# Performance work log

Hardware: AMD Instinct MI355X
Metric: run time of the kernel (lower is better)

Reference implementation:

```python
import jax, jax.numpy as jnp
import numpy as np

TAU = 1.0  # forward() default temperature

def setup_inputs() -> dict:
    key = jax.random.key(0)
    ks = jax.random.split(key, 6)
    B, T, I, H, O = 1024, 512, 100, 150, 3
    s_ih = 1.0 / np.sqrt(H)  # torch nn.RNN init scale (uniform +-1/sqrt(H)); randn used for simplicity of magnitude
    return {
        "x": jax.random.normal(ks[0], (B, T, I), dtype=jnp.float32),
        "h0": jax.random.normal(ks[1], (B, H), dtype=jnp.float32),  # init=True: h ~ N(0,1)
        "g": jax.random.normal(ks[2], (B, T, O), dtype=jnp.float32),  # gumbel noise (externalized)
        "W_ih": jax.random.normal(ks[3], (H, I), dtype=jnp.float32) * s_ih,
        "W_hh": jax.random.normal(ks[4], (H, H), dtype=jnp.float32) * s_ih,
        "W_fc": jax.random.normal(ks[5], (O, H), dtype=jnp.float32) * s_ih,
    }

def _rnn_relu(x, h0, W_ih, W_hh):
    # x: [B,T,I]; precompute input projection once (batched GEMM), then scan over time.
    xw = jnp.einsum("bti,hi->tbh", x, W_ih)  # [T,B,H]
    def step(h, xw_t):
        h = jax.nn.relu(xw_t + h @ W_hh.T)
        return h, h
    _, hs = jax.lax.scan(step, h0, xw)  # hs: [T,B,H]
    return jnp.transpose(hs, (1, 0, 2))  # [B,T,H]

def reference(x, h0, g, W_ih, W_hh, W_fc):
    hidden = _rnn_relu(x, h0, W_ih, W_hh)           # [B,T,H]
    logits = jnp.einsum("bth,oh->bto", hidden, W_fc)  # [B,T,O]
    # F.gumbel_softmax(hard=True): softmax((logits+g)/tau), straight-through one-hot
    y_soft = jax.nn.softmax((logits + g) / TAU, axis=-1)
    idx = jnp.argmax(y_soft, axis=-1)
    y_hard = jax.nn.one_hot(idx, logits.shape[-1], dtype=y_soft.dtype)
    out = y_soft + jax.lax.stop_gradient(y_hard - y_soft)
    return (out, hidden, logits)
```

## Files before the change

### kernel.cpp

```cpp
#include <hip/hip_runtime.h>

constexpr int NB = 1024;
constexpr int NT = 512;
constexpr int NI = 100;
constexpr int NH = 150;
constexpr int NO = 3;
constexpr int KP = 256;
constexpr int XOFF = 152;
constexpr int ROWS = 4;
constexpr int NCH = 8;

__global__ __launch_bounds__(512, 2)
void rnn_fused(const float* __restrict__ x, const float* __restrict__ h0,
               const float* __restrict__ g, const float* __restrict__ Wih,
               const float* __restrict__ Whh, const float* __restrict__ Wfc,
               float* __restrict__ out, float* __restrict__ hidden,
               float* __restrict__ logits)
{
    __shared__ __align__(16) float hx[ROWS * KP];
    __shared__ float lgt[ROWS][4];

    const int tid  = threadIdx.x;
    const int lane = tid & 63;
    const int wv   = tid >> 6;
    const int kg   = lane & 7;
    const int oq   = lane >> 3;
    const int oi   = wv * 8 + oq;
    const int row0 = blockIdx.x * ROWS;

    float Wreg[3][NCH][4];
#pragma unroll
    for (int j = 0; j < 3; ++j) {
        const int o = oi + 64 * j;
#pragma unroll
        for (int i = 0; i < NCH; ++i) {
#pragma unroll
            for (int q = 0; q < 4; ++q) {
                const int k = 4 * (kg + 8 * i) + q;
                float v = 0.f;
                if (o < NH) {
                    if (k < NH) v = Whh[o * NH + k];
                    else if (k >= XOFF && k < XOFF + NI) v = Wih[o * NI + (k - XOFF)];
                } else if (o < NH + NO) {
                    if (k < NH) v = Wfc[(o - NH) * NH + k];
                }
                Wreg[j][i][q] = v;
            }
        }
    }

    for (int e = tid; e < ROWS * NH; e += 512) {
        int b = e / NH, k = e - b * NH;
        hx[b * KP + k] = h0[(row0 + b) * NH + k];
    }
    for (int e = tid; e < ROWS * NI; e += 512) {
        int b = e / NI, i = e - b * NI;
        hx[b * KP + XOFF + i] = x[((size_t)(row0 + b) * NT + 0) * NI + i];
    }
    if (tid < ROWS * 6) {
        int b = tid / 6, z = tid - b * 6;
        int k = (z < 2) ? (NH + z) : (252 + z - 2);
        hx[b * KP + k] = 0.f;
    }
    __syncthreads();

    const float4* hx4 = reinterpret_cast<const float4*>(hx);
    const int xb = tid / 25, xq = tid - xb * 25;

    for (int t = 0; t <= NT; ++t) {
        float4 xp = make_float4(0.f, 0.f, 0.f, 0.f);
        if (tid < 100 && t < NT - 1) {
            xp = *reinterpret_cast<const float4*>(
                &x[((size_t)(row0 + xb) * NT + (t + 1)) * NI + 4 * xq]);
        }
        float g0 = 0.f, g1 = 0.f, g2 = 0.f;
        if (tid < ROWS && t >= 1) {
            const float* gp = &g[((size_t)(row0 + tid) * NT + (t - 1)) * NO];
            g0 = gp[0]; g1 = gp[1]; g2 = gp[2];
        }

        float acc[3][ROWS];
#pragma unroll
        for (int j = 0; j < 3; ++j)
#pragma unroll
            for (int b = 0; b < ROWS; ++b) acc[j][b] = 0.f;

#pragma unroll
        for (int i = 0; i < NCH; ++i) {
            const int c = kg + 8 * i;
#pragma unroll
            for (int b = 0; b < ROWS; ++b) {
                const float4 hv = hx4[b * (KP / 4) + c];
#pragma unroll
                for (int j = 0; j < 3; ++j) {
                    acc[j][b] += Wreg[j][i][0] * hv.x;
                    acc[j][b] += Wreg[j][i][1] * hv.y;
                    acc[j][b] += Wreg[j][i][2] * hv.z;
                    acc[j][b] += Wreg[j][i][3] * hv.w;
                }
            }
        }

#pragma unroll
        for (int m = 1; m <= 4; m <<= 1) {
#pragma unroll
            for (int j = 0; j < 3; ++j)
#pragma unroll
                for (int b = 0; b < ROWS; ++b)
                    acc[j][b] += __shfl_xor(acc[j][b], m);
        }

        __syncthreads();

        if (kg == 0) {
#pragma unroll
            for (int j = 0; j < 3; ++j) {
                const int o = oi + 64 * j;
                if (o < NH) {
                    if (t < NT) {
#pragma unroll
                        for (int b = 0; b < ROWS; ++b) {
                            float v = fmaxf(acc[j][b], 0.f);
                            hx[b * KP + o] = v;
                            hidden[((size_t)(row0 + b) * NT + t) * NH + o] = v;
                        }
                    }
                } else if (o < NH + NO) {
#pragma unroll
                    for (int b = 0; b < ROWS; ++b) lgt[b][o - NH] = acc[j][b];
                }
            }
        }
        if (tid < 100 && t < NT - 1) {
            *reinterpret_cast<float4*>(&hx[xb * KP + XOFF + 4 * xq]) = xp;
        }
        __syncthreads();

        if (tid < ROWS && t >= 1) {
            float l0 = lgt[tid][0], l1 = lgt[tid][1], l2 = lgt[tid][2];
            float s0 = l0 + g0, s1 = l1 + g1, s2 = l2 + g2;
            int am = 0; float best = s0;
            if (s1 > best) { best = s1; am = 1; }
            if (s2 > best) { am = 2; }
            size_t base = ((size_t)(row0 + tid) * NT + (t - 1)) * NO;
            out[base + 0] = (am == 0) ? 1.f : 0.f;
            out[base + 1] = (am == 1) ? 1.f : 0.f;
            out[base + 2] = (am == 2) ? 1.f : 0.f;
            logits[base + 0] = l0;
            logits[base + 1] = l1;
            logits[base + 2] = l2;
        }
    }
}

extern "C" void kernel_launch(void* const* d_in, const int* in_sizes, int n_in,
                              void* d_out, int out_size, void* d_ws, size_t ws_size,
                              hipStream_t stream) {
    const float* x   = (const float*)d_in[0];
    const float* h0  = (const float*)d_in[1];
    const float* g   = (const float*)d_in[2];
    const float* Wih = (const float*)d_in[3];
    const float* Whh = (const float*)d_in[4];
    const float* Wfc = (const float*)d_in[5];

    float* out    = (float*)d_out;
    float* hidden = out + (size_t)NB * NT * NO;
    float* logits = hidden + (size_t)NB * NT * NH;

    hipLaunchKernelGGL(rnn_fused, dim3(NB / ROWS), dim3(512), 0, stream,
                       x, h0, g, Wih, Whh, Wfc, out, hidden, logits);
}
```

Measured before the change: 1.522 ms.

## Double-buffer hidden state to drop a barrier and use DPP reductions

Splits the shared hidden/input buffer into two ping-pong buffers, so each timestep reads one and writes the other. That removes one of the two __syncthreads per step. It also replaces the shfl_xor butterfly reduction with DPP row operations, and spreads the per-row writeback across lanes kg<4 instead of having kg==0 do all four rows. The risk is the correctness of the DPP control codes: after the ops, every lane in the group of 8 must hold the full sum. The larger shared footprint could also affect occupancy slightly.

```diff
diff --git a/kernel.cpp b/kernel.cpp
--- a/kernel.cpp
+++ b/kernel.cpp
@@ -10,6 +10,12 @@
 constexpr int ROWS = 4;
 constexpr int NCH = 8;
 
+template<int CTRL>
+__device__ __forceinline__ float dpp_add(float v) {
+    int t = __builtin_amdgcn_update_dpp(0, __float_as_int(v), CTRL, 0xF, 0xF, true);
+    return v + __int_as_float(t);
+}
+
 __global__ __launch_bounds__(512, 2)
 void rnn_fused(const float* __restrict__ x, const float* __restrict__ h0,
                const float* __restrict__ g, const float* __restrict__ Wih,
@@ -17,8 +23,8 @@
                float* __restrict__ out, float* __restrict__ hidden,
                float* __restrict__ logits)
 {
-    __shared__ __align__(16) float hx[ROWS * KP];
-    __shared__ float lgt[ROWS][4];
+    __shared__ __align__(16) float hx[2][ROWS * KP];
+    __shared__ float lg[2][ROWS][4];
 
     const int tid  = threadIdx.x;
     const int lane = tid & 63;
@@ -51,34 +57,39 @@
 
     for (int e = tid; e < ROWS * NH; e += 512) {
         int b = e / NH, k = e - b * NH;
-        hx[b * KP + k] = h0[(row0 + b) * NH + k];
+        hx[0][b * KP + k] = h0[(row0 + b) * NH + k];
     }
     for (int e = tid; e < ROWS * NI; e += 512) {
         int b = e / NI, i = e - b * NI;
-        hx[b * KP + XOFF + i] = x[((size_t)(row0 + b) * NT + 0) * NI + i];
+        hx[0][b * KP + XOFF + i] = x[((size_t)(row0 + b) * NT + 0) * NI + i];
     }
-    if (tid < ROWS * 6) {
-        int b = tid / 6, z = tid - b * 6;
+    if (tid < 2 * ROWS * 6) {
+        int u = tid; int f = u / (ROWS * 6); u -= f * (ROWS * 6);
+        int b = u / 6, z = u - b * 6;
         int k = (z < 2) ? (NH + z) : (252 + z - 2);
-        hx[b * KP + k] = 0.f;
+        hx[f][b * KP + k] = 0.f;
     }
     __syncthreads();
 
-    const float4* hx4 = reinterpret_cast<const float4*>(hx);
     const int xb = tid / 25, xq = tid - xb * 25;
+    const float* xrow = x + ((size_t)(row0 + (xb & 3)) * NT) * NI + 4 * xq;
+    float* hidb = hidden + ((size_t)(row0 + (kg & 3)) * NT) * NH;
+    const float* grow = g + ((size_t)(row0 + (tid & 3)) * NT) * NO;
+    const size_t emitb = ((size_t)(row0 + (tid & 3)) * NT) * NO;
 
-    for (int t = 0; t <= NT; ++t) {
+    auto step = [&](int t, const float* __restrict__ cur, float* __restrict__ nxt,
+                    float (*__restrict__ lgb)[4]) {
         float4 xp = make_float4(0.f, 0.f, 0.f, 0.f);
-        if (tid < 100 && t < NT - 1) {
-            xp = *reinterpret_cast<const float4*>(
-                &x[((size_t)(row0 + xb) * NT + (t + 1)) * NI + 4 * xq]);
-        }
+        const bool do_x = (tid < 100) && (t < NT - 1);
+        if (do_x) xp = *reinterpret_cast<const float4*>(xrow + (size_t)(t + 1) * NI);
         float g0 = 0.f, g1 = 0.f, g2 = 0.f;
-        if (tid < ROWS && t >= 1) {
-            const float* gp = &g[((size_t)(row0 + tid) * NT + (t - 1)) * NO];
+        const bool do_e = (tid < ROWS) && (t >= 1);
+        if (do_e) {
+            const float* gp = grow + (size_t)(t - 1) * NO;
             g0 = gp[0]; g1 = gp[1]; g2 = gp[2];
         }
 
+        const float4* cur4 = reinterpret_cast<const float4*>(cur);
         float acc[3][ROWS];
 #pragma unroll
         for (int j = 0; j < 3; ++j)
@@ -90,7 +101,7 @@
             const int c = kg + 8 * i;
 #pragma unroll
             for (int b = 0; b < ROWS; ++b) {
-                const float4 hv = hx4[b * (KP / 4) + c];
+                const float4 hv = cur4[b * (KP / 4) + c];
 #pragma unroll
                 for (int j = 0; j < 3; ++j) {
                     acc[j][b] += Wreg[j][i][0] * hv.x;
@@ -102,47 +113,42 @@
         }
 
 #pragma unroll
-        for (int m = 1; m <= 4; m <<= 1) {
+        for (int j = 0; j < 3; ++j)
 #pragma unroll
-            for (int j = 0; j < 3; ++j)
-#pragma unroll
-                for (int b = 0; b < ROWS; ++b)
-                    acc[j][b] += __shfl_xor(acc[j][b], m);
-        }
+            for (int b = 0; b < ROWS; ++b) {
+                float v = acc[j][b];
+                v = dpp_add<0xB1>(v);
+                v = dpp_add<0x4E>(v);
+                v = dpp_add<0x141>(v);
+                acc[j][b] = v;
+            }
 
-        __syncthreads();
-
-        if (kg == 0) {
+        if (kg < ROWS) {
+            const int b = kg;
 #pragma unroll
             for (int j = 0; j < 3; ++j) {
                 const int o = oi + 64 * j;
                 if (o < NH) {
                     if (t < NT) {
-#pragma unroll
-                        for (int b = 0; b < ROWS; ++b) {
-                            float v = fmaxf(acc[j][b], 0.f);
-                            hx[b * KP + o] = v;
-                            hidden[((size_t)(row0 + b) * NT + t) * NH + o] = v;
-                        }
+                        float v = fmaxf(acc[j][b], 0.f);
+                        nxt[b * KP + o] = v;
+                        hidb[(size_t)t * NH + o] = v;
                     }
                 } else if (o < NH + NO) {
-#pragma unroll
-                    for (int b = 0; b < ROWS; ++b) lgt[b][o - NH] = acc[j][b];
+                    lgb[b][o - NH] = acc[j][b];
                 }
             }
         }
-        if (tid < 100 && t < NT - 1) {
-            *reinterpret_cast<float4*>(&hx[xb * KP + XOFF + 4 * xq]) = xp;
-        }
+        if (do_x) *reinterpret_cast<float4*>(nxt + xb * KP + XOFF + 4 * xq) = xp;
         __syncthreads();
 
-        if (tid < ROWS && t >= 1) {
-            float l0 = lgt[tid][0], l1 = lgt[tid][1], l2 = lgt[tid][2];
+        if (do_e) {
+            float l0 = lgb[tid][0], l1 = lgb[tid][1], l2 = lgb[tid][2];
             float s0 = l0 + g0, s1 = l1 + g1, s2 = l2 + g2;
             int am = 0; float best = s0;
             if (s1 > best) { best = s1; am = 1; }
             if (s2 > best) { am = 2; }
-            size_t base = ((size_t)(row0 + tid) * NT + (t - 1)) * NO;
+            size_t base = emitb + (size_t)(t - 1) * NO;
             out[base + 0] = (am == 0) ? 1.f : 0.f;
             out[base + 1] = (am == 1) ? 1.f : 0.f;
             out[base + 2] = (am == 2) ? 1.f : 0.f;
@@ -150,7 +156,13 @@
             logits[base + 1] = l1;
             logits[base + 2] = l2;
         }
+    };
+
+    for (int t = 0; t < NT; t += 2) {
+        step(t,     hx[0], hx[1], lg[0]);
+        step(t + 1, hx[1], hx[0], lg[1]);
     }
+    step(NT, hx[0], hx[1], lg[0]);
 }
 
 extern "C" void kernel_launch(void* const* d_in, const int* in_sizes, int n_in,
```

After: 1.512 ms. No clear change (-0.7%).
